# Performance work log

Hardware: AMD Instinct MI355X
Metric: run time of the kernel (lower is better)

The kernel has to match this reference:

```python
import jax, jax.numpy as jnp
import numpy as np

N_NODES = 102400
N_EDGES = 1638400
IN_SIZE = 128
OUT_SIZE = 128
G_SIZE = 100


def setup_inputs() -> dict:
    key = jax.random.key(0)
    ks = jax.random.split(key, 8)
    x = jax.random.normal(ks[0], (N_NODES, IN_SIZE), dtype=jnp.float32)
    W1 = jax.random.normal(ks[1], (IN_SIZE, OUT_SIZE), dtype=jnp.float32) * (IN_SIZE ** -0.5)
    b1 = jnp.zeros((OUT_SIZE,), dtype=jnp.float32)
    W2 = jax.random.normal(ks[2], (OUT_SIZE, OUT_SIZE), dtype=jnp.float32) * (OUT_SIZE ** -0.5)
    b2 = jnp.zeros((OUT_SIZE,), dtype=jnp.float32)
    W3 = jax.random.normal(ks[3], (OUT_SIZE, OUT_SIZE), dtype=jnp.float32) * (OUT_SIZE ** -0.5)
    b3 = jnp.zeros((OUT_SIZE,), dtype=jnp.float32)
    edge_src = jax.random.randint(ks[4], (N_EDGES,), 0, N_NODES, dtype=jnp.int64)
    edge_dst = jax.random.randint(ks[5], (N_EDGES,), 0, N_NODES, dtype=jnp.int64)
    return {"x": x, "W1": W1, "b1": b1, "W2": W2, "b2": b2, "W3": W3, "b3": b3,
            "edge_src": edge_src, "edge_dst": edge_dst, "g_size": G_SIZE}


def _degree_norm(idx, n_nodes):
    # DGL norm='both': deg.clamp(min=1) ** -0.5
    deg = jax.ops.segment_sum(jnp.ones(idx.shape, dtype=jnp.float32), idx, num_segments=n_nodes)
    return jnp.maximum(deg, 1.0) ** -0.5  # [N]


def _graph_conv(feat, W, b, edge_src, edge_dst, src_norm, dst_norm):
    # out = D_dst^{-1/2} A (D_src^{-1/2} feat) W + b
    h = feat * src_norm[:, None]                                   # [N, d]
    agg = jax.ops.segment_sum(h[edge_src], edge_dst, num_segments=feat.shape[0])  # SpMM gather+scatter
    agg = agg * dst_norm[:, None]
    return agg @ W + b


def reference(x, W1, b1, W2, b2, W3, b3, edge_src, edge_dst, g_size):
    n = x.shape[0]
    src_norm = _degree_norm(edge_src, n)  # out-degree based
    dst_norm = _degree_norm(edge_dst, n)  # in-degree based

    y1 = jax.nn.elu(_graph_conv(x, W1, b1, edge_src, edge_dst, src_norm, dst_norm))
    y2 = jax.nn.elu(_graph_conv(y1, W2, b2, edge_src, edge_dst, src_norm, dst_norm))
    y3 = jax.nn.softmax(_graph_conv(y2, W3, b3, edge_src, edge_dst, src_norm, dst_norm), axis=1)

    d = y1.shape[-1]
    return (y1.reshape(-1, g_size, d), y2.reshape(-1, g_size, d), y3.reshape(-1, g_size, d))
```

## Files before the change

kernel.cpp:

```cpp
#include <hip/hip_runtime.h>
#include <hip/hip_fp16.h>
#include <cstdint>
#include <cstddef>

#define N_NODES 102400
#define N_EDGES 1638400
#define DIM 128
#define SLOTS 48
#define NB 200
#define BKT_CAP 9216
#define SC_BLOCKS 400
#define SC_EPT 16

typedef _Float16 f16x8 __attribute__((ext_vector_type(8)));
typedef float f32x4 __attribute__((ext_vector_type(4)));


__global__ void k_initcur(int* __restrict__ dstCur, int* __restrict__ srcCur,
                          unsigned short* __restrict__ fbA,
                          unsigned short* __restrict__ fbB) {
  const int i = threadIdx.x;
  if (i < NB) {
    dstCur[i] = i * BKT_CAP;
    srcCur[i] = i * BKT_CAP;
  }
  if (i < 64) {
    reinterpret_cast<unsigned*>(fbA + (size_t)N_NODES * DIM)[i] = 0u;
  } else if (i < 128) {
    reinterpret_cast<unsigned*>(fbB + (size_t)N_NODES * DIM)[i - 64] = 0u;
  }
}

__global__ void k_cvt_w(const float* __restrict__ W1,
                        const float* __restrict__ W2,
                        const float* __restrict__ W3,
                        _Float16* __restrict__ Wt) {
  const int i = blockIdx.x * 256 + threadIdx.x;
  const int w = i >> 14;
  const int r = i & 16383;
  const int col = r >> 7;
  const int k = r & 127;
  const float* W = (w == 0) ? W1 : ((w == 1) ? W2 : W3);
  Wt[i] = (_Float16)W[k * DIM + col];
}

__global__ __launch_bounds__(256) void k_scatter(
    const int* __restrict__ esrc, const int* __restrict__ edst,
    int* __restrict__ dstCur, int* __restrict__ srcCur,
    unsigned* __restrict__ dstStage, unsigned short* __restrict__ srcStage) {
  __shared__ int histD[NB], histS[NB], baseD[NB], baseS[NB], locD[NB], locS[NB];
  const int tid = threadIdx.x;
  const int ebase = blockIdx.x * (256 * SC_EPT);

  for (int i = tid; i < NB; i += 256) {
    histD[i] = 0; histS[i] = 0; locD[i] = 0; locS[i] = 0;
  }
  __syncthreads();

  int s[SC_EPT], d[SC_EPT];
  #pragma unroll
  for (int k = 0; k < SC_EPT; ++k) {
    const int e = ebase + k * 256 + tid;
    s[k] = esrc[e];
    d[k] = edst[e];
    atomicAdd(&histD[d[k] >> 9], 1);
    atomicAdd(&histS[s[k] >> 9], 1);
  }
  __syncthreads();

  for (int i = tid; i < NB; i += 256) {
    baseD[i] = atomicAdd(&dstCur[i], histD[i]);
    baseS[i] = atomicAdd(&srcCur[i], histS[i]);
  }
  __syncthreads();

  #pragma unroll
  for (int k = 0; k < SC_EPT; ++k) {
    const int bd = d[k] >> 9;
    const int od = atomicAdd(&locD[bd], 1);
    dstStage[baseD[bd] + od] = ((unsigned)s[k] << 9) | (unsigned)(d[k] & 511);
    const int bs = s[k] >> 9;
    const int os = atomicAdd(&locS[bs], 1);
    srcStage[baseS[bs] + os] = (unsigned short)(s[k] & 511);
  }
}

__global__ __launch_bounds__(256) void k_csr(
    const unsigned* __restrict__ dstStage, const int* __restrict__ dstCur,
    const unsigned short* __restrict__ srcStage, const int* __restrict__ srcCur,
    int* __restrict__ cnt, unsigned* __restrict__ csr,
    int* __restrict__ deg_src) {
  __shared__ int c[512], cur[512], cs[512];
  const int b = blockIdx.x;
  const int tid = threadIdx.x;
  const int node0 = b * 512;

  const unsigned dummy = (unsigned)N_NODES << 8;
  uint4 dv;
  dv.x = dummy; dv.y = dummy; dv.z = dummy; dv.w = dummy;
  uint4* c4 = reinterpret_cast<uint4*>(csr + (size_t)node0 * SLOTS);
  for (int i = tid; i < 512 * SLOTS / 4; i += 256) c4[i] = dv;

  #pragma unroll
  for (int k = 0; k < 2; ++k) {
    c[tid + k * 256] = 0;
    cur[tid + k * 256] = 0;
    cs[tid + k * 256] = 0;
  }
  __syncthreads();

  const int base = b * BKT_CAP;
  const int n = dstCur[b] - base;
  for (int i = tid; i < n; i += 256) {
    atomicAdd(&c[dstStage[base + i] & 511], 1);
  }
  const int ns = srcCur[b] - base;
  for (int i = tid; i < ns; i += 256) {
    atomicAdd(&cs[srcStage[base + i]], 1);
  }
  __syncthreads();

  #pragma unroll
  for (int k = 0; k < 2; ++k) {
    cnt[node0 + tid + k * 256] = c[tid + k * 256];
    deg_src[node0 + tid + k * 256] = cs[tid + k * 256];
  }

  for (int i = tid; i < n; i += 256) {
    const unsigned e = dstStage[base + i];
    const int dloc = (int)(e & 511u);
    const int slot = atomicAdd(&cur[dloc], 1);
    csr[(size_t)(node0 + dloc) * SLOTS + slot] = (e >> 9) << 8;
  }
}

__global__ void k_cvt_scale(const float* __restrict__ x,
                            const int* __restrict__ deg_src,
                            unsigned short* __restrict__ out) {
  const int i = blockIdx.x * blockDim.x + threadIdx.x;
  const int row = i >> 5;
  const int dg = deg_src[row];
  const float sn = rsqrtf((float)(dg > 0 ? dg : 1));
  const float4 v = reinterpret_cast<const float4*>(x)[i];
  ushort4 o;
  o.x = __half_as_ushort(__float2half_rn(v.x * sn));
  o.y = __half_as_ushort(__float2half_rn(v.y * sn));
  o.z = __half_as_ushort(__float2half_rn(v.z * sn));
  o.w = __half_as_ushort(__float2half_rn(v.w * sn));
  reinterpret_cast<ushort4*>(out)[i] = o;
}

template <int ACT>
__global__ __launch_bounds__(256, 8) void k_layer_m(
    const unsigned short* __restrict__ fb_in, const _Float16* __restrict__ Wt,
    const float* __restrict__ bias, const int* __restrict__ cnt,
    const unsigned* __restrict__ csr, const int* __restrict__ deg_src,
    float* __restrict__ out, unsigned short* __restrict__ fb_out) {
  __shared__ float buf[32][132];
  __half* aggH = reinterpret_cast<__half*>(&buf[0][0]);

  const int tid  = threadIdx.x;
  const int lane = tid & 63;
  const int wid  = tid >> 6;
  const int q    = lane >> 4;
  const int li   = lane & 15;
  const int brow = blockIdx.x * 32;
  const char* fbase = reinterpret_cast<const char*>(fb_in);

  int c_[8];
  unsigned pk_[8];
  #pragma unroll
  for (int k = 0; k < 8; ++k) {
    const int gr = brow + wid + 4 * k;
    c_[k] = cnt[gr];
    pk_[k] = (lane < SLOTS) ? csr[(size_t)gr * SLOTS + lane] : 0u;
  }

  #pragma unroll
  for (int pass = 0; pass < 2; ++pass) {
    const int kb = pass * 4;
    __half2 acc[4][4];
    #pragma unroll
    for (int k = 0; k < 4; ++k)
      #pragma unroll
      for (int i = 0; i < 4; ++i) acc[k][i] = __float2half2_rn(0.0f);

    int cmax = c_[kb] > c_[kb + 1] ? c_[kb] : c_[kb + 1];
    cmax = cmax > c_[kb + 2] ? cmax : c_[kb + 2];
    cmax = cmax > c_[kb + 3] ? cmax : c_[kb + 3];
    cmax = cmax > SLOTS ? SLOTS : cmax;
    const int nq = (cmax + 3) >> 2;

    #pragma unroll 2
    for (int j = 0; j < nq; ++j) {
      const int sl = 4 * j + q;
      #pragma unroll
      for (int k = 0; k < 4; ++k) {
        const int o = __shfl((int)pk_[kb + k], sl);
        const uint4 v = *reinterpret_cast<const uint4*>(
            fbase + (size_t)(unsigned)o + (li << 4));
        acc[k][0] = __hadd2(acc[k][0], *reinterpret_cast<const __half2*>(&v.x));
        acc[k][1] = __hadd2(acc[k][1], *reinterpret_cast<const __half2*>(&v.y));
        acc[k][2] = __hadd2(acc[k][2], *reinterpret_cast<const __half2*>(&v.z));
        acc[k][3] = __hadd2(acc[k][3], *reinterpret_cast<const __half2*>(&v.w));
      }
    }

    #pragma unroll
    for (int k = 0; k < 4; ++k) {
      #pragma unroll
      for (int i = 0; i < 4; ++i) {
        int t = __shfl_xor(*reinterpret_cast<int*>(&acc[k][i]), 32);
        acc[k][i] = __hadd2(acc[k][i], *reinterpret_cast<__half2*>(&t));
        t = __shfl_xor(*reinterpret_cast<int*>(&acc[k][i]), 16);
        acc[k][i] = __hadd2(acc[k][i], *reinterpret_cast<__half2*>(&t));
      }
      if (q == 0) {
        const int cc = c_[kb + k];
        const __half2 dn = __float2half2_rn(rsqrtf((float)(cc > 0 ? cc : 1)));
        uint4 s;
        __half2 h;
        h = __hmul2(acc[k][0], dn); s.x = *reinterpret_cast<unsigned*>(&h);
        h = __hmul2(acc[k][1], dn); s.y = *reinterpret_cast<unsigned*>(&h);
        h = __hmul2(acc[k][2], dn); s.z = *reinterpret_cast<unsigned*>(&h);
        h = __hmul2(acc[k][3], dn); s.w = *reinterpret_cast<unsigned*>(&h);
        *reinterpret_cast<uint4*>(
            aggH + (size_t)(wid + 4 * (kb + k)) * 136 + li * 8) = s;
      }
    }
  }
  __syncthreads();

  f32x4 acc00 = {0.f, 0.f, 0.f, 0.f};
  f32x4 acc01 = {0.f, 0.f, 0.f, 0.f};
  f32x4 acc10 = {0.f, 0.f, 0.f, 0.f};
  f32x4 acc11 = {0.f, 0.f, 0.f, 0.f};
  const int colbase = wid * 32 + li;
  const _Float16* wt0 = Wt + (size_t)colbase * DIM;

  #pragma unroll
  for (int kc = 0; kc < 4; ++kc) {
    const int k0 = kc * 32 + q * 8;
    const f16x8 a0 = *reinterpret_cast<const f16x8*>(aggH + (size_t)li * 136 + k0);
    const f16x8 a1 =
        *reinterpret_cast<const f16x8*>(aggH + (size_t)(16 + li) * 136 + k0);
    const f16x8 b0 = *reinterpret_cast<const f16x8*>(wt0 + k0);
    const f16x8 b1 = *reinterpret_cast<const f16x8*>(wt0 + 16 * DIM + k0);
    acc00 = __builtin_amdgcn_mfma_f32_16x16x32_f16(a0, b0, acc00, 0, 0, 0);
    acc01 = __builtin_amdgcn_mfma_f32_16x16x32_f16(a0, b1, acc01, 0, 0, 0);
    acc10 = __builtin_amdgcn_mfma_f32_16x16x32_f16(a1, b0, acc10, 0, 0, 0);
    acc11 = __builtin_amdgcn_mfma_f32_16x16x32_f16(a1, b1, acc11, 0, 0, 0);
  }
  __syncthreads();

  #pragma unroll
  for (int r = 0; r < 4; ++r) {
    const int row0 = q * 4 + r;
    buf[row0][colbase] = acc00[r];
    buf[row0][colbase + 16] = acc01[r];
    buf[row0 + 16][colbase] = acc10[r];
    buf[row0 + 16][colbase + 16] = acc11[r];
  }
  __syncthreads();

  const int tc = tid & 31;
  const int tr = tid >> 5;
  const int c0 = tc << 2;
  const float4 bv = *reinterpret_cast<const float4*>(bias + c0);
  #pragma unroll
  for (int i = 0; i < 4; ++i) {
    const int row = tr * 4 + i;
    float4 v = *reinterpret_cast<const float4*>(&buf[row][c0]);
    v.x += bv.x; v.y += bv.y; v.z += bv.z; v.w += bv.w;
    if (ACT == 0) {
      v.x = v.x > 0.f ? v.x : expm1f(v.x);
      v.y = v.y > 0.f ? v.y : expm1f(v.y);
      v.z = v.z > 0.f ? v.z : expm1f(v.z);
      v.w = v.w > 0.f ? v.w : expm1f(v.w);
    } else {
      float m = fmaxf(fmaxf(v.x, v.y), fmaxf(v.z, v.w));
      #pragma unroll
      for (int off = 16; off >= 1; off >>= 1) m = fmaxf(m, __shfl_xor(m, off));
      v.x = expf(v.x - m);
      v.y = expf(v.y - m);
      v.z = expf(v.z - m);
      v.w = expf(v.w - m);
      float s = v.x + v.y + v.z + v.w;
      #pragma unroll
      for (int off = 16; off >= 1; off >>= 1) s += __shfl_xor(s, off);
      const float inv = 1.0f / s;
      v.x *= inv; v.y *= inv; v.z *= inv; v.w *= inv;
    }
    const size_t grow = (size_t)(brow + row);
    *reinterpret_cast<float4*>(out + grow * DIM + c0) = v;
    if (ACT == 0 && fb_out != nullptr) {
      const int dg = deg_src[grow];
      const float sn = rsqrtf((float)(dg > 0 ? dg : 1));
      ushort4 o;
      o.x = __half_as_ushort(__float2half_rn(v.x * sn));
      o.y = __half_as_ushort(__float2half_rn(v.y * sn));
      o.z = __half_as_ushort(__float2half_rn(v.z * sn));
      o.w = __half_as_ushort(__float2half_rn(v.w * sn));
      *reinterpret_cast<ushort4*>(fb_out + grow * DIM + c0) = o;
    }
  }
}

__global__ void k_dummyfill(unsigned* __restrict__ csr,
                            unsigned short* __restrict__ fbA,
                            unsigned short* __restrict__ fbB) {
  const unsigned dummy = (unsigned)N_NODES << 8;
  uint4 dv;
  dv.x = dummy; dv.y = dummy; dv.z = dummy; dv.w = dummy;
  const int i = blockIdx.x * blockDim.x + threadIdx.x;
  if (i < N_NODES * SLOTS / 4) reinterpret_cast<uint4*>(csr)[i] = dv;
  if (i < 64) reinterpret_cast<unsigned*>(fbA + (size_t)N_NODES * DIM)[i] = 0u;
  else if (i < 128)
    reinterpret_cast<unsigned*>(fbB + (size_t)N_NODES * DIM)[i - 64] = 0u;
}

__global__ void k_build(const int* __restrict__ esrc, const int* __restrict__ edst,
                        int* __restrict__ deg_src, int* __restrict__ cnt,
                        unsigned* __restrict__ csr) {
  const int i = blockIdx.x * blockDim.x + threadIdx.x;
  if (i < N_EDGES) {
    const int s = esrc[i];
    const int d = edst[i];
    atomicAdd(&deg_src[s], 1);
    const int pos = atomicAdd(&cnt[d], 1);
    csr[(size_t)d * SLOTS + pos] = (unsigned)s << 8;
  }
}

static inline size_t align1k(size_t x) { return (x + 1023) & ~(size_t)1023; }

extern "C" void kernel_launch(void* const* d_in, const int* in_sizes, int n_in,
                              void* d_out, int out_size, void* d_ws,
                              size_t ws_size, hipStream_t stream) {
  const float* x  = (const float*)d_in[0];
  const float* W1 = (const float*)d_in[1];
  const float* b1 = (const float*)d_in[2];
  const float* W2 = (const float*)d_in[3];
  const float* b2 = (const float*)d_in[4];
  const float* W3 = (const float*)d_in[5];
  const float* b3 = (const float*)d_in[6];
  const int* esrc = (const int*)d_in[7];
  const int* edst = (const int*)d_in[8];

  float* y1 = (float*)d_out;
  float* y2 = y1 + (size_t)N_NODES * DIM;
  float* y3 = y2 + (size_t)N_NODES * DIM;

  const size_t fb_bytes = (size_t)(N_NODES + 1) * DIM * 2;

  {
    char* ws = (char*)d_ws;
    int* dstCur = (int*)ws;                 ws += align1k(NB * 4);
    int* srcCur = (int*)ws;                 ws += align1k(NB * 4);
    _Float16* Wt3 = (_Float16*)ws;          ws += align1k(3 * 16384 * 2);
    int* cnt = (int*)ws;                    ws += align1k((size_t)N_NODES * 4);
    int* deg_src = (int*)ws;                ws += align1k((size_t)N_NODES * 4);
    unsigned* csr = (unsigned*)ws;          ws += align1k((size_t)N_NODES * SLOTS * 4);
    unsigned* dstStage = (unsigned*)ws;     ws += align1k((size_t)NB * BKT_CAP * 4);
    unsigned short* srcStage = (unsigned short*)ws;
                                            ws += align1k((size_t)NB * BKT_CAP * 2);
    unsigned short* fbA = (unsigned short*)ws;  ws += align1k(fb_bytes);
    unsigned short* fbB = (unsigned short*)ws;  ws += align1k(fb_bytes);
    const size_t need_v2 = (size_t)(ws - (char*)d_ws);

    if (ws_size >= need_v2) {
      k_initcur<<<1, 256, 0, stream>>>(dstCur, srcCur, fbA, fbB);
      k_cvt_w<<<192, 256, 0, stream>>>(W1, W2, W3, Wt3);
      k_scatter<<<SC_BLOCKS, 256, 0, stream>>>(esrc, edst, dstCur, srcCur,
                                               dstStage, srcStage);
      k_csr<<<NB, 256, 0, stream>>>(dstStage, dstCur, srcStage, srcCur, cnt,
                                    csr, deg_src);
      k_cvt_scale<<<N_NODES * DIM / 4 / 256, 256, 0, stream>>>(x, deg_src, fbA);

      k_layer_m<0><<<N_NODES / 32, 256, 0, stream>>>(
          fbA, Wt3, b1, cnt, csr, deg_src, y1, fbB);
      k_layer_m<0><<<N_NODES / 32, 256, 0, stream>>>(
          fbB, Wt3 + 16384, b2, cnt, csr, deg_src, y2, fbA);
      k_layer_m<1><<<N_NODES / 32, 256, 0, stream>>>(
          fbA, Wt3 + 32768, b3, cnt, csr, deg_src, y3, nullptr);
      return;
    }
  }

  {
    char* ws = (char*)d_ws;
    int* cnt     = (int*)ws;  ws += (size_t)N_NODES * 4;
    int* deg_src = (int*)ws;  ws += (size_t)N_NODES * 4;
    _Float16* Wt3 = (_Float16*)ws;  ws += align1k(3 * 16384 * 2);
    unsigned* csr = (unsigned*)ws;  ws += (size_t)N_NODES * SLOTS * 4;
    unsigned short* fbA = (unsigned short*)ws;  ws += align1k(fb_bytes);
    unsigned short* fbB = (unsigned short*)ws;  ws += align1k(fb_bytes);

    (void)hipMemsetAsync(cnt, 0, (size_t)N_NODES * 2 * sizeof(int), stream);
    k_dummyfill<<<(N_NODES * SLOTS / 4 + 255) / 256, 256, 0, stream>>>(csr, fbA,
                                                                       fbB);
    k_cvt_w<<<192, 256, 0, stream>>>(W1, W2, W3, Wt3);
    k_build<<<(N_EDGES + 255) / 256, 256, 0, stream>>>(esrc, edst, deg_src,
                                                       cnt, csr);
    k_cvt_scale<<<N_NODES * DIM / 4 / 256, 256, 0, stream>>>(x, deg_src, fbA);

    k_layer_m<0><<<N_NODES / 32, 256, 0, stream>>>(
        fbA, Wt3, b1, cnt, csr, deg_src, y1, fbB);
    k_layer_m<0><<<N_NODES / 32, 256, 0, stream>>>(
        fbB, Wt3 + 16384, b2, cnt, csr, deg_src, y2, fbA);
    k_layer_m<1><<<N_NODES / 32, 256, 0, stream>>>(
        fbA, Wt3 + 32768, b3, cnt, csr, deg_src, y3, nullptr);
  }
}
```

Measured before the change: 300.4 us.

## Group each node's CSR neighbours by source range and rotate groups per XCD

```diff
diff --git a/kernel.cpp b/kernel.cpp
--- a/kernel.cpp
+++ b/kernel.cpp
@@ -11,6 +11,7 @@
 #define BKT_CAP 9216
 #define SC_BLOCKS 400
 #define SC_EPT 16
+#define NGRP 8
 
 typedef _Float16 f16x8 __attribute__((ext_vector_type(8)));
 typedef float f32x4 __attribute__((ext_vector_type(4)));
@@ -89,48 +90,52 @@
     const unsigned* __restrict__ dstStage, const int* __restrict__ dstCur,
     const unsigned short* __restrict__ srcStage, const int* __restrict__ srcCur,
     int* __restrict__ cnt, unsigned* __restrict__ csr,
-    int* __restrict__ deg_src) {
-  __shared__ int c[512], cur[512], cs[512];
+    unsigned long long* __restrict__ grpOff, int* __restrict__ deg_src) {
+  __shared__ int c[512 * NGRP];
+  __shared__ int cur[512 * NGRP];
+  __shared__ int cs[512];
   const int b = blockIdx.x;
   const int tid = threadIdx.x;
   const int node0 = b * 512;
 
-  const unsigned dummy = (unsigned)N_NODES << 8;
-  uint4 dv;
-  dv.x = dummy; dv.y = dummy; dv.z = dummy; dv.w = dummy;
-  uint4* c4 = reinterpret_cast<uint4*>(csr + (size_t)node0 * SLOTS);
-  for (int i = tid; i < 512 * SLOTS / 4; i += 256) c4[i] = dv;
-
-  #pragma unroll
-  for (int k = 0; k < 2; ++k) {
-    c[tid + k * 256] = 0;
-    cur[tid + k * 256] = 0;
-    cs[tid + k * 256] = 0;
-  }
+  for (int i = tid; i < 512 * NGRP; i += 256) c[i] = 0;
+  for (int i = tid; i < 512; i += 256) cs[i] = 0;
   __syncthreads();
 
   const int base = b * BKT_CAP;
   const int n = dstCur[b] - base;
   for (int i = tid; i < n; i += 256) {
-    atomicAdd(&c[dstStage[base + i] & 511], 1);
+    const unsigned e = dstStage[base + i];
+    const int dloc = (int)(e & 511u);
+    const int g = (int)((e >> 18) / 25u);
+    atomicAdd(&c[dloc * NGRP + g], 1);
   }
   const int ns = srcCur[b] - base;
-  for (int i = tid; i < ns; i += 256) {
-    atomicAdd(&cs[srcStage[base + i]], 1);
-  }
-  __syncthreads();
-
-  #pragma unroll
-  for (int k = 0; k < 2; ++k) {
-    cnt[node0 + tid + k * 256] = c[tid + k * 256];
-    deg_src[node0 + tid + k * 256] = cs[tid + k * 256];
-  }
+  for (int i = tid; i < ns; i += 256) atomicAdd(&cs[srcStage[base + i]], 1);
+  __syncthreads();
+
+  for (int nl = tid; nl < 512; nl += 256) {
+    int off = 0;
+    unsigned long long go = 0ull;
+    #pragma unroll
+    for (int g = 0; g < NGRP; ++g) {
+      go |= (unsigned long long)(unsigned)(off > 255 ? 255 : off) << (8 * g);
+      cur[nl * NGRP + g] = off;
+      off += c[nl * NGRP + g];
+    }
+    cnt[node0 + nl] = off;
+    grpOff[node0 + nl] = go;
+    deg_src[node0 + nl] = cs[nl];
+  }
+  __syncthreads();
 
   for (int i = tid; i < n; i += 256) {
     const unsigned e = dstStage[base + i];
     const int dloc = (int)(e & 511u);
-    const int slot = atomicAdd(&cur[dloc], 1);
-    csr[(size_t)(node0 + dloc) * SLOTS + slot] = (e >> 9) << 8;
+    const int g = (int)((e >> 18) / 25u);
+    const int slot = atomicAdd(&cur[dloc * NGRP + g], 1);
+    if (slot < SLOTS)
+      csr[(size_t)(node0 + dloc) * SLOTS + slot] = (e >> 9) << 8;
   }
 }
 
@@ -151,11 +156,13 @@
 }
 
 template <int ACT>
-__global__ __launch_bounds__(256, 8) void k_layer_m(
+__global__ __launch_bounds__(256, 6) void k_layer_m(
     const unsigned short* __restrict__ fb_in, const _Float16* __restrict__ Wt,
     const float* __restrict__ bias, const int* __restrict__ cnt,
-    const unsigned* __restrict__ csr, const int* __restrict__ deg_src,
-    float* __restrict__ out, unsigned short* __restrict__ fb_out) {
+    const unsigned* __restrict__ csr,
+    const unsigned long long* __restrict__ grpOff,
+    const int* __restrict__ deg_src, float* __restrict__ out,
+    unsigned short* __restrict__ fb_out) {
   __shared__ float buf[32][132];
   __half* aggH = reinterpret_cast<__half*>(&buf[0][0]);
 
@@ -165,44 +172,62 @@
   const int q    = lane >> 4;
   const int li   = lane & 15;
   const int brow = blockIdx.x * 32;
+  const int xcd  = blockIdx.x & 7;
   const char* fbase = reinterpret_cast<const char*>(fb_in);
+  const unsigned dummyOff = (unsigned)N_NODES << 8;
 
   int c_[8];
   unsigned pk_[8];
   #pragma unroll
   for (int k = 0; k < 8; ++k) {
     const int gr = brow + wid + 4 * k;
-    c_[k] = cnt[gr];
+    int cc = cnt[gr];
+    c_[k] = cc > SLOTS ? SLOTS : cc;
     pk_[k] = (lane < SLOTS) ? csr[(size_t)gr * SLOTS + lane] : 0u;
   }
 
   #pragma unroll
   for (int pass = 0; pass < 2; ++pass) {
     const int kb = pass * 4;
+    unsigned long long go[4];
+    #pragma unroll
+    for (int k = 0; k < 4; ++k)
+      go[k] = grpOff[brow + wid + 4 * (kb + k)];
+
     __half2 acc[4][4];
     #pragma unroll
     for (int k = 0; k < 4; ++k)
       #pragma unroll
       for (int i = 0; i < 4; ++i) acc[k][i] = __float2half2_rn(0.0f);
 
-    int cmax = c_[kb] > c_[kb + 1] ? c_[kb] : c_[kb + 1];
-    cmax = cmax > c_[kb + 2] ? cmax : c_[kb + 2];
-    cmax = cmax > c_[kb + 3] ? cmax : c_[kb + 3];
-    cmax = cmax > SLOTS ? SLOTS : cmax;
-    const int nq = (cmax + 3) >> 2;
-
-    #pragma unroll 2
-    for (int j = 0; j < nq; ++j) {
-      const int sl = 4 * j + q;
+    for (int rot = 0; rot < NGRP; ++rot) {
+      const int gg = (xcd + rot) & 7;
+      int o0[4], o1[4];
+      int nmax = 0;
       #pragma unroll
       for (int k = 0; k < 4; ++k) {
-        const int o = __shfl((int)pk_[kb + k], sl);
-        const uint4 v = *reinterpret_cast<const uint4*>(
-            fbase + (size_t)(unsigned)o + (li << 4));
-        acc[k][0] = __hadd2(acc[k][0], *reinterpret_cast<const __half2*>(&v.x));
-        acc[k][1] = __hadd2(acc[k][1], *reinterpret_cast<const __half2*>(&v.y));
-        acc[k][2] = __hadd2(acc[k][2], *reinterpret_cast<const __half2*>(&v.z));
-        acc[k][3] = __hadd2(acc[k][3], *reinterpret_cast<const __half2*>(&v.w));
+        o0[k] = (int)((go[k] >> (8 * gg)) & 0xFFull);
+        o1[k] = (gg < 7) ? (int)((go[k] >> (8 * gg + 8)) & 0xFFull)
+                         : c_[kb + k];
+        o1[k] = o1[k] > c_[kb + k] ? c_[kb + k] : o1[k];
+        const int len = o1[k] - o0[k];
+        nmax = len > nmax ? len : nmax;
+      }
+      const int nq = (nmax + 3) >> 2;
+
+      for (int j = 0; j < nq; ++j) {
+        #pragma unroll
+        for (int k = 0; k < 4; ++k) {
+          const int sl = o0[k] + 4 * j + q;
+          const unsigned off = (unsigned)__shfl((int)pk_[kb + k], sl & 63);
+          const unsigned a = (sl < o1[k]) ? off : dummyOff;
+          const uint4 v = *reinterpret_cast<const uint4*>(
+              fbase + (size_t)a + (li << 4));
+          acc[k][0] = __hadd2(acc[k][0], *reinterpret_cast<const __half2*>(&v.x));
+          acc[k][1] = __hadd2(acc[k][1], *reinterpret_cast<const __half2*>(&v.y));
+          acc[k][2] = __hadd2(acc[k][2], *reinterpret_cast<const __half2*>(&v.z));
+          acc[k][3] = __hadd2(acc[k][3], *reinterpret_cast<const __half2*>(&v.w));
+        }
       }
     }
 
@@ -306,19 +331,6 @@
   }
 }
 
-__global__ void k_dummyfill(unsigned* __restrict__ csr,
-                            unsigned short* __restrict__ fbA,
-                            unsigned short* __restrict__ fbB) {
-  const unsigned dummy = (unsigned)N_NODES << 8;
-  uint4 dv;
-  dv.x = dummy; dv.y = dummy; dv.z = dummy; dv.w = dummy;
-  const int i = blockIdx.x * blockDim.x + threadIdx.x;
-  if (i < N_NODES * SLOTS / 4) reinterpret_cast<uint4*>(csr)[i] = dv;
-  if (i < 64) reinterpret_cast<unsigned*>(fbA + (size_t)N_NODES * DIM)[i] = 0u;
-  else if (i < 128)
-    reinterpret_cast<unsigned*>(fbB + (size_t)N_NODES * DIM)[i - 64] = 0u;
-}
-
 __global__ void k_build(const int* __restrict__ esrc, const int* __restrict__ edst,
                         int* __restrict__ deg_src, int* __restrict__ cnt,
                         unsigned* __restrict__ csr) {
@@ -328,7 +340,19 @@
     const int d = edst[i];
     atomicAdd(&deg_src[s], 1);
     const int pos = atomicAdd(&cnt[d], 1);
-    csr[(size_t)d * SLOTS + pos] = (unsigned)s << 8;
+    if (pos < SLOTS) csr[(size_t)d * SLOTS + pos] = (unsigned)s << 8;
+  }
+}
+
+__global__ void k_goff(const int* __restrict__ cnt,
+                       unsigned long long* __restrict__ grpOff) {
+  const int i = blockIdx.x * 256 + threadIdx.x;
+  if (i < N_NODES) {
+    unsigned long long cc = (unsigned long long)(unsigned)(cnt[i] > 255 ? 255 : cnt[i]);
+    unsigned long long go = 0ull;
+    #pragma unroll
+    for (int g = 1; g < NGRP; ++g) go |= cc << (8 * g);
+    grpOff[i] = go;
   }
 }
 
@@ -360,6 +384,8 @@
     _Float16* Wt3 = (_Float16*)ws;          ws += align1k(3 * 16384 * 2);
     int* cnt = (int*)ws;                    ws += align1k((size_t)N_NODES * 4);
     int* deg_src = (int*)ws;                ws += align1k((size_t)N_NODES * 4);
+    unsigned long long* grpOff = (unsigned long long*)ws;
+                                            ws += align1k((size_t)N_NODES * 8);
     unsigned* csr = (unsigned*)ws;          ws += align1k((size_t)N_NODES * SLOTS * 4);
     unsigned* dstStage = (unsigned*)ws;     ws += align1k((size_t)NB * BKT_CAP * 4);
     unsigned short* srcStage = (unsigned short*)ws;
@@ -374,41 +400,45 @@
       k_scatter<<<SC_BLOCKS, 256, 0, stream>>>(esrc, edst, dstCur, srcCur,
                                                dstStage, srcStage);
       k_csr<<<NB, 256, 0, stream>>>(dstStage, dstCur, srcStage, srcCur, cnt,
-                                    csr, deg_src);
+                                    csr, grpOff, deg_src);
       k_cvt_scale<<<N_NODES * DIM / 4 / 256, 256, 0, stream>>>(x, deg_src, fbA);
 
       k_layer_m<0><<<N_NODES / 32, 256, 0, stream>>>(
-          fbA, Wt3, b1, cnt, csr, deg_src, y1, fbB);
+          fbA, Wt3, b1, cnt, csr, grpOff, deg_src, y1, fbB);
       k_layer_m<0><<<N_NODES / 32, 256, 0, stream>>>(
-          fbB, Wt3 + 16384, b2, cnt, csr, deg_src, y2, fbA);
+          fbB, Wt3 + 16384, b2, cnt, csr, grpOff, deg_src, y2, fbA);
       k_layer_m<1><<<N_NODES / 32, 256, 0, stream>>>(
-          fbA, Wt3 + 32768, b3, cnt, csr, deg_src, y3, nullptr);
+          fbA, Wt3 + 32768, b3, cnt, csr, grpOff, deg_src, y3, nullptr);
       return;
     }
   }
 
   {
     char* ws = (char*)d_ws;
+    int* dstCur = (int*)ws;   ws += align1k(NB * 4);
+    int* srcCur = (int*)ws;   ws += align1k(NB * 4);
     int* cnt     = (int*)ws;  ws += (size_t)N_NODES * 4;
     int* deg_src = (int*)ws;  ws += (size_t)N_NODES * 4;
     _Float16* Wt3 = (_Float16*)ws;  ws += align1k(3 * 16384 * 2);
+    unsigned long long* grpOff = (unsigned long long*)ws;
+                              ws += align1k((size_t)N_NODES * 8);
     unsigned* csr = (unsigned*)ws;  ws += (size_t)N_NODES * SLOTS * 4;
     unsigned short* fbA = (unsigned short*)ws;  ws += align1k(fb_bytes);
     unsigned short* fbB = (unsigned short*)ws;  ws += align1k(fb_bytes);
 
     (void)hipMemsetAsync(cnt, 0, (size_t)N_NODES * 2 * sizeof(int), stream);
-    k_dummyfill<<<(N_NODES * SLOTS / 4 + 255) / 256, 256, 0, stream>>>(csr, fbA,
-                                                                       fbB);
+    k_initcur<<<1, 256, 0, stream>>>(dstCur, srcCur, fbA, fbB);
     k_cvt_w<<<192, 256, 0, stream>>>(W1, W2, W3, Wt3);
     k_build<<<(N_EDGES + 255) / 256, 256, 0, stream>>>(esrc, edst, deg_src,
                                                        cnt, csr);
+    k_goff<<<(N_NODES + 255) / 256, 256, 0, stream>>>(cnt, grpOff);
     k_cvt_scale<<<N_NODES * DIM / 4 / 256, 256, 0, stream>>>(x, deg_src, fbA);
 
     k_layer_m<0><<<N_NODES / 32, 256, 0, stream>>>(
-        fbA, Wt3, b1, cnt, csr, deg_src, y1, fbB);
+        fbA, Wt3, b1, cnt, csr, grpOff, deg_src, y1, fbB);
     k_layer_m<0><<<N_NODES / 32, 256, 0, stream>>>(
-        fbB, Wt3 + 16384, b2, cnt, csr, deg_src, y2, fbA);
+        fbB, Wt3 + 16384, b2, cnt, csr, grpOff, deg_src, y2, fbA);
     k_layer_m<1><<<N_NODES / 32, 256, 0, stream>>>(
-        fbA, Wt3 + 32768, b3, cnt, csr, deg_src, y3, nullptr);
-  }
-}
+        fbA, Wt3 + 32768, b3, cnt, csr, grpOff, deg_src, y3, nullptr);
+  }
+}
```

Result: slower. 344.7 us (+14.8%).
